# Performance work log

Measured on AMD Instinct MI355X. Metric: run time of the kernel, lower is better.

## Reference

```python
import jax, jax.numpy as jnp
import numpy as np

B, C, H, W = 8, 512, 32, 32
NH = 8


def setup_inputs() -> dict:
    key = jax.random.key(0)
    ks = jax.random.split(key, 10)
    s = 1.0 / np.sqrt(C)
    return {
        "query": jax.random.normal(ks[0], (B, C, H, W), jnp.float32),
        "key": jax.random.normal(ks[1], (B, C, H, W), jnp.float32),
        "Wq": jax.random.normal(ks[2], (C, C), jnp.float32) * s,
        "bq": jnp.zeros((C,), jnp.float32),
        "Wk": jax.random.normal(ks[3], (C, C), jnp.float32) * s,
        "bk": jnp.zeros((C,), jnp.float32),
        "Wv": jax.random.normal(ks[4], (C, C), jnp.float32) * s,
        "bv": jnp.zeros((C,), jnp.float32),
        "Wo": jax.random.normal(ks[5], (C, C), jnp.float32) * s,
        "bo": jnp.zeros((C,), jnp.float32),
        "num_heads": NH,
    }


def reference(query, key, Wq, bq, Wk, bk, Wv, bv, Wo, bo, num_heads):
    b, c, h, w = query.shape
    hd = c // num_heads
    scale = hd ** (-0.5)
    # [B,C,H,W] -> [B, L, C] with L = H*W
    qf = jnp.transpose(query, (0, 2, 3, 1)).reshape(b, -1, c)
    kf = jnp.transpose(key, (0, 2, 3, 1)).reshape(b, -1, c)
    L = qf.shape[1]
    # Linear projections (torch Linear: x @ W.T + b); value = key
    q = qf @ Wq.T + bq
    k = kf @ Wk.T + bk
    v = kf @ Wv.T + bv
    # split heads: [B, L, NH, hd] -> [B, NH, L, hd]
    q = q.reshape(b, L, num_heads, hd).transpose(0, 2, 1, 3) * scale
    k = k.reshape(b, L, num_heads, hd).transpose(0, 2, 1, 3)
    v = v.reshape(b, L, num_heads, hd).transpose(0, 2, 1, 3)
    scores = jnp.einsum('bhqd,bhkd->bhqk', q, k)
    attn = jax.nn.softmax(scores, axis=-1)  # dropout p=0.0 -> identity
    o = jnp.einsum('bhqk,bhkd->bhqd', attn, v)
    o = o.transpose(0, 2, 1, 3).reshape(b, L, c)
    o = o @ Wo.T + bo
    o = o + qf + kf  # residual with flattened query and key
    return jnp.transpose(o.reshape(b, h, w, c), (0, 3, 1, 2))
```

## Files before the change

### kernel.cpp

```cpp
#include <hip/hip_runtime.h>
#include <stdint.h>

#define B_  8
#define C_  512
#define L_  1024
#define NH_ 8
#define HD_ 64

typedef __attribute__((ext_vector_type(8))) short short8;
typedef __attribute__((ext_vector_type(4))) short short4v;
typedef __attribute__((ext_vector_type(4))) float f32x4;
typedef __attribute__((ext_vector_type(2))) unsigned uint2v;

#define MFMA(a,b,c) __builtin_amdgcn_mfma_f32_16x16x32_bf16((a),(b),(c),0,0,0)
#define GLD16(g,l) __builtin_amdgcn_global_load_lds( \
    (const __attribute__((address_space(1))) void*)(g), \
    (__attribute__((address_space(3))) void*)(l), 16, 0, 0)

__device__ __forceinline__ unsigned short f2bf(float f) {
  union { float f; unsigned u; } x; x.f = f;
  unsigned r = x.u + 0x7FFFu + ((x.u >> 16) & 1u);
  return (unsigned short)(r >> 16);
}

__device__ __forceinline__ unsigned cvtpk_bf16(float lo, float hi) {
  unsigned r;
  asm("v_cvt_pk_bf16_f32 %0, %1, %2" : "=v"(r) : "v"(lo), "v"(hi));
  return r;
}

__global__ __launch_bounds__(256) void k_transpose(
    const float* __restrict__ q, const float* __restrict__ k,
    unsigned short* __restrict__ qf, unsigned short* __restrict__ kf,
    const float* __restrict__ w0, const float* __restrict__ w1,
    const float* __restrict__ w2, const float* __restrict__ w3,
    unsigned short* __restrict__ wdst) {
  const int z = blockIdx.z;
  if (z == 16) {
    const int gb = blockIdx.y * 32 + blockIdx.x;
    const float* s = (gb < 128) ? w0 : (gb < 256) ? w1 : (gb < 384) ? w2 : w3;
    const int off = (gb & 127) * 2048 + threadIdx.x * 8;
    float4 v0 = *(const float4*)&s[off];
    float4 v1 = *(const float4*)&s[off + 4];
    short8 p;
    p[0] = (short)f2bf(v0.x); p[1] = (short)f2bf(v0.y);
    p[2] = (short)f2bf(v0.z); p[3] = (short)f2bf(v0.w);
    p[4] = (short)f2bf(v1.x); p[5] = (short)f2bf(v1.y);
    p[6] = (short)f2bf(v1.z); p[7] = (short)f2bf(v1.w);
    *(short8*)&wdst[(size_t)(gb >> 7) * 262144 + off] = p;
    return;
  }
  __shared__ float t[32][33];
  const int b = z >> 1;
  const float* src = (z & 1) ? k : q;
  unsigned short* dst = (z & 1) ? kf : qf;
  const int tx = threadIdx.x & 31;
  const int ty = threadIdx.x >> 5;
  const int l0 = blockIdx.x * 32;
  const int c0 = blockIdx.y * 32;
#pragma unroll
  for (int i = 0; i < 4; ++i)
    t[ty + 8*i][tx] = src[((size_t)b * C_ + c0 + ty + 8*i) * L_ + l0 + tx];
  __syncthreads();
#pragma unroll
  for (int i = 0; i < 4; ++i)
    dst[((size_t)b * L_ + l0 + ty + 8*i) * C_ + c0 + tx] = f2bf(t[tx][ty + 8*i]);
}

template<int MREP>
__device__ __forceinline__ void gemm_core(
    const unsigned short* __restrict__ A, const unsigned short* __restrict__ W,
    const float* __restrict__ bias, void* __restrict__ outp,
    const float* __restrict__ resQ, const float* __restrict__ resK,
    int mode, float scale, unsigned short* lA, unsigned short* lB,
    int tm, int tn) {
  const int lane = threadIdx.x & 63;
  const int wid  = threadIdx.x >> 6;
  const int wm = wid >> 1, wn = wid & 1;
  const int r16 = lane & 15;
  const int g4  = lane >> 4;

  f32x4 acc[MREP][4];
#pragma unroll
  for (int i = 0; i < MREP; ++i)
#pragma unroll
    for (int j = 0; j < 4; ++j) acc[i][j] = (f32x4){0.f, 0.f, 0.f, 0.f};

  for (int kt = 0; kt < C_; kt += 64) {
#pragma unroll
    for (int i = 0; i < MREP; ++i) {
      int chunk = wid * MREP + i;
      int row = chunk * 8 + (lane >> 3);
      int col = (lane & 7) * 8;
      GLD16(A + (size_t)(tm + row) * C_ + kt + col, &lA[chunk * 512]);
    }
#pragma unroll
    for (int i = 0; i < 4; ++i) {
      int chunk = wid * 4 + i;
      int row = chunk * 8 + (lane >> 3);
      int col = (lane & 7) * 8;
      GLD16(W + (size_t)(tn + row) * C_ + kt + col, &lB[chunk * 512]);
    }
    __syncthreads();
#pragma unroll
    for (int ks = 0; ks < 2; ++ks) {
      const int co = ks * 32 + g4 * 8;
      short8 af[MREP], bw[4];
#pragma unroll
      for (int i = 0; i < MREP; ++i)
        af[i] = *(const short8*)&lA[(wm*(MREP*16) + i*16 + r16) * 64 + co];
#pragma unroll
      for (int j = 0; j < 4; ++j) bw[j] = *(const short8*)&lB[(wn*64 + j*16 + r16) * 64 + co];
#pragma unroll
      for (int i = 0; i < MREP; ++i)
#pragma unroll
        for (int j = 0; j < 4; ++j) acc[i][j] = MFMA(af[i], bw[j], acc[i][j]);
    }
    __syncthreads();
  }

  if (mode <= 1) {
    unsigned short* out = (unsigned short*)outp;
#pragma unroll
    for (int i = 0; i < MREP; ++i)
#pragma unroll
      for (int j = 0; j < 4; ++j) {
        int c = tn + wn*64 + j*16 + r16;
        float bia = bias[c];
        int h = c >> 6, d = c & 63;
#pragma unroll
        for (int r = 0; r < 4; ++r) {
          int gm = tm + wm*(MREP*16) + i*16 + g4*4 + r;
          int b = gm >> 10, l = gm & 1023;
          out[(((size_t)b * NH_ + h) * L_ + l) * HD_ + d] = f2bf((acc[i][j][r] + bia) * scale);
        }
      }
  } else if (mode == 2) {
    unsigned short* out = (unsigned short*)outp;
#pragma unroll
    for (int i = 0; i < MREP; ++i)
#pragma unroll
      for (int j = 0; j < 4; ++j) {
        int c = tn + wn*64 + j*16 + r16;
        float bia = bias[c];
        int h = c >> 6, d = c & 63;
        int gm0 = tm + wm*(MREP*16) + i*16 + g4*4;
        int b = gm0 >> 10, l0 = gm0 & 1023;
        short4v pk;
#pragma unroll
        for (int r = 0; r < 4; ++r) pk[r] = (short)f2bf(acc[i][j][r] + bia);
        *(short4v*)&out[(((size_t)b * NH_ + h) * HD_ + d) * L_ + l0] = pk;
      }
  } else {
    float* out = (float*)outp;
#pragma unroll
    for (int i = 0; i < MREP; ++i)
#pragma unroll
      for (int j = 0; j < 4; ++j) {
        int c = tn + wn*64 + j*16 + r16;
        float bia = bias[c];
        int gm0 = tm + wm*(MREP*16) + i*16 + g4*4;
        int b = gm0 >> 10, l0 = gm0 & 1023;
        size_t idx = ((size_t)b * C_ + c) * L_ + l0;
        float4 q4 = *(const float4*)&resQ[idx];
        float4 k4 = *(const float4*)&resK[idx];
        float4 o4;
        o4.x = acc[i][j][0] + bia + q4.x + k4.x;
        o4.y = acc[i][j][1] + bia + q4.y + k4.y;
        o4.z = acc[i][j][2] + bia + q4.z + k4.z;
        o4.w = acc[i][j][3] + bia + q4.w + k4.w;
        *(float4*)&out[idx] = o4;
      }
  }
}

__global__ __launch_bounds__(256) void k_proj(
    const unsigned short* __restrict__ qf, const unsigned short* __restrict__ kf,
    const unsigned short* __restrict__ Wqb, const unsigned short* __restrict__ Wkb,
    const unsigned short* __restrict__ Wvb,
    const float* __restrict__ bq, const float* __restrict__ bk, const float* __restrict__ bv,
    unsigned short* __restrict__ Qw, unsigned short* __restrict__ Kw,
    unsigned short* __restrict__ VTw) {
  __shared__ unsigned short lA[128 * 64];
  __shared__ unsigned short lB[128 * 64];
  const int bid = blockIdx.x;
  const int xcd = bid & 7;
  const int i_  = bid >> 3;
  const int ml  = i_ / 12;
  const int rem = i_ - ml * 12;
  const int z   = rem >> 2;
  const int n   = rem & 3;
  const int m   = xcd * 8 + ml;
  const unsigned short* A = (z == 0) ? qf : kf;
  const unsigned short* W = (z == 0) ? Wqb : (z == 1) ? Wkb : Wvb;
  const float* bias = (z == 0) ? bq : (z == 1) ? bk : bv;
  void* out = (z == 0) ? (void*)Qw : (z == 1) ? (void*)Kw : (void*)VTw;
  float scale = (z == 0) ? 0.125f * 1.44269504088896f : 1.0f;
  gemm_core<4>(A, W, bias, out, nullptr, nullptr, z, scale, lA, lB, m * 128, n * 128);
}

__global__ __launch_bounds__(256) void k_outproj(
    const unsigned short* __restrict__ O, const unsigned short* __restrict__ Wob,
    const float* __restrict__ bo, float* __restrict__ out,
    const float* __restrict__ query, const float* __restrict__ key) {
  __shared__ unsigned short lA[64 * 64];
  __shared__ unsigned short lB[128 * 64];
  const int bid = blockIdx.x;
  const int xcd = bid & 7;
  const int i_  = bid >> 3;
  const int m   = xcd * 16 + (i_ >> 2);
  const int n   = i_ & 3;
  gemm_core<2>(O, Wob, bo, out, query, key, 3, 1.0f, lA, lB, m * 64, n * 128);
}

__global__ __launch_bounds__(256, 2) void k_attn(
    const unsigned short* __restrict__ Q, const unsigned short* __restrict__ K,
    const unsigned short* __restrict__ VT, unsigned short* __restrict__ O) {
  __shared__ unsigned short Kt[2][64 * 64];
  __shared__ unsigned short Vt[2][64 * 64];
  const int lane = threadIdx.x & 63;
  const int wid  = threadIdx.x >> 6;
  const int bid  = blockIdx.x;
  const int xcd  = bid & 7;
  const int i_   = bid >> 3;
  const int bh   = xcd * 8 + (i_ >> 3);
  const int qb   = i_ & 7;
  const int qrow0 = qb * 128 + wid * 32;
  const int r16 = lane & 15;
  const int g4  = lane >> 4;
  const size_t base = (size_t)bh * L_ * HD_;
  const unsigned short* Kg = K + base;
  const unsigned short* Vg = VT + base;

  const int s0 = wid * 128 + lane;
  const int row0 = s0 >> 3,        ch0 = (s0 & 7) ^ (row0 & 7);
  const int row1 = (s0 + 64) >> 3, ch1 = ((s0 + 64) & 7) ^ (row1 & 7);

#define STAGE_KV(nxt, kt0) { \
    GLD16(Kg + (size_t)((kt0) + row0) * HD_ + ch0 * 8, &Kt[nxt][(wid*128)*8]); \
    GLD16(Kg + (size_t)((kt0) + row1) * HD_ + ch1 * 8, &Kt[nxt][(wid*128+64)*8]); \
    GLD16(Vg + (size_t)row0 * L_ + (kt0) + ch0 * 8, &Vt[nxt][(wid*128)*8]); \
    GLD16(Vg + (size_t)row1 * L_ + (kt0) + ch1 * 8, &Vt[nxt][(wid*128+64)*8]); \
  }

  short8 qv[2][2];
#pragma unroll
  for (int i = 0; i < 2; ++i)
#pragma unroll
    for (int ks = 0; ks < 2; ++ks)
      qv[i][ks] = *(const short8*)(Q + base + (size_t)(qrow0 + i*16 + r16) * HD_ + ks*32 + g4*8);

  short8 vones;
#pragma unroll
  for (int e = 0; e < 8; ++e) vones[e] = (short)0x3F80;

  f32x4 lacc[2];
  f32x4 oacc[2][4];
#pragma unroll
  for (int i = 0; i < 2; ++i) {
    lacc[i] = (f32x4){0.f, 0.f, 0.f, 0.f};
#pragma unroll
    for (int j = 0; j < 4; ++j) oacc[i][j] = (f32x4){0.f, 0.f, 0.f, 0.f};
  }

  STAGE_KV(0, 0);
  __syncthreads();

  int cur = 0;
  for (int t = 0; t < 16; ++t) {
    if (t < 15) STAGE_KV(cur ^ 1, (t + 1) * 64);

    const unsigned short* lK = &Kt[cur][0];
    const unsigned short* lV = &Vt[cur][0];

    f32x4 sc[2][4];
#pragma unroll
    for (int i = 0; i < 2; ++i)
#pragma unroll
      for (int cf = 0; cf < 4; ++cf) sc[i][cf] = (f32x4){0.f, 0.f, 0.f, 0.f};

    __builtin_amdgcn_s_setprio(1);
#pragma unroll
    for (int cf = 0; cf < 4; ++cf) {
      const int h = cf >> 1, c = cf & 1;
      const int rr = h*32 + ((r16 >> 2) << 3) + ((r16 & 3) << 1) + c;
      const int s  = ((r16 & 3) << 1) + c;
      const int rowb = rr * 64;
      short8 kb0 = *(const short8*)&lK[rowb + ((g4) ^ s) * 8];
      short8 kb1 = *(const short8*)&lK[rowb + ((4 + g4) ^ s) * 8];
      sc[0][cf] = MFMA(kb0, qv[0][0], sc[0][cf]);
      sc[0][cf] = MFMA(kb1, qv[0][1], sc[0][cf]);
      sc[1][cf] = MFMA(kb0, qv[1][0], sc[1][cf]);
      sc[1][cf] = MFMA(kb1, qv[1][1], sc[1][cf]);
    }
    __builtin_amdgcn_s_setprio(0);

    const int swz = r16 & 7;
#pragma unroll
    for (int h = 0; h < 2; ++h) {
      union { unsigned u[4]; short8 s8; } pu0, pu1;
#pragma unroll
      for (int r = 0; r < 4; ++r) {
        pu0.u[r] = cvtpk_bf16(exp2f(sc[0][h*2][r]), exp2f(sc[0][h*2+1][r]));
        pu1.u[r] = cvtpk_bf16(exp2f(sc[1][h*2][r]), exp2f(sc[1][h*2+1][r]));
      }
      short8 pa0 = pu0.s8;
      short8 pa1 = pu1.s8;
      __builtin_amdgcn_s_setprio(1);
      lacc[0] = MFMA(pa0, vones, lacc[0]);
      lacc[1] = MFMA(pa1, vones, lacc[1]);
#pragma unroll
      for (int j = 0; j < 4; ++j) {
        short8 vb = *(const short8*)&lV[(j*16 + r16) * 64 + ((h*4 + g4) ^ swz) * 8];
        oacc[0][j] = MFMA(pa0, vb, oacc[0][j]);
        oacc[1][j] = MFMA(pa1, vb, oacc[1][j]);
      }
      __builtin_amdgcn_s_setprio(0);
    }

    __syncthreads();
    cur ^= 1;
  }

  const int b = bh >> 3, h = bh & 7;
#pragma unroll
  for (int i = 0; i < 2; ++i) {
    float linv[4];
#pragma unroll
    for (int r = 0; r < 4; ++r) linv[r] = 1.0f / lacc[i][r];
#pragma unroll
    for (int j = 0; j < 4; ++j)
#pragma unroll
      for (int r = 0; r < 4; ++r) {
        int row = qrow0 + i*16 + g4*4 + r;
        int col = h*64 + j*16 + r16;
        O[((size_t)b * L_ + row) * C_ + col] = f2bf(oacc[i][j][r] * linv[r]);
      }
  }
#undef STAGE_KV
}

extern "C" void kernel_launch(void* const* d_in, const int* in_sizes, int n_in,
                              void* d_out, int out_size, void* d_ws, size_t ws_size,
                              hipStream_t stream) {
  (void)in_sizes; (void)n_in; (void)out_size; (void)ws_size;
  const float* query = (const float*)d_in[0];
  const float* key   = (const float*)d_in[1];
  const float* Wq = (const float*)d_in[2];
  const float* bq = (const float*)d_in[3];
  const float* Wk = (const float*)d_in[4];
  const float* bk = (const float*)d_in[5];
  const float* Wv = (const float*)d_in[6];
  const float* bv = (const float*)d_in[7];
  const float* Wo = (const float*)d_in[8];
  const float* bo = (const float*)d_in[9];

  char* ws = (char*)d_ws;
  unsigned short* qf  = (unsigned short*)(ws);
  unsigned short* kf  = (unsigned short*)(ws + 8388608);
  unsigned short* Wqb = (unsigned short*)(ws + 16777216);
  unsigned short* Wkb = Wqb + 262144;
  unsigned short* Wvb = Wkb + 262144;
  unsigned short* Wob = Wvb + 262144;
  unsigned short* Qw  = (unsigned short*)(ws + 18874368);
  unsigned short* Kw  = (unsigned short*)(ws + 27262976);
  unsigned short* VTw = (unsigned short*)(ws + 35651584);
  unsigned short* Ow  = (unsigned short*)(ws + 44040192);

  k_transpose<<<dim3(32, 16, 17), 256, 0, stream>>>(query, key, qf, kf,
                                                    Wq, Wk, Wv, Wo, Wqb);
  k_proj<<<dim3(768), 256, 0, stream>>>(qf, kf, Wqb, Wkb, Wvb, bq, bk, bv, Qw, Kw, VTw);
  k_attn<<<dim3(512), 256, 0, stream>>>(Qw, Kw, VTw, Ow);
  k_outproj<<<dim3(512), 256, 0, stream>>>(Ow, Wob, bo, (float*)d_out, query, key);
}
```

Before: 93.04 us.

## Double-buffer GEMM LDS tiles with swizzled layout and prefetch next K-slice

```diff
diff --git a/kernel.cpp b/kernel.cpp
--- a/kernel.cpp
+++ b/kernel.cpp
@@ -80,44 +80,64 @@
   const int r16 = lane & 15;
   const int g4  = lane >> 4;
 
+  constexpr int ASLOTS = MREP * 128;
+  constexpr int BSLOTS = 512;
+
+  const int sB0 = wid * 128 + lane;
+  const int rB0 = sB0 >> 2;
+  const int cB0 = (sB0 & 3) ^ ((rB0 >> 1) & 3);
+  const int sA0 = wid * (ASLOTS / 4) + lane;
+  const int rA0 = sA0 >> 2;
+  const int cA0 = (sA0 & 3) ^ ((rA0 >> 1) & 3);
+
+#define G_STAGE(bb, kt) { \
+    if constexpr (MREP == 4) { \
+      GLD16(A + (size_t)(tm + rA0) * C_ + (kt) + cA0 * 8, &lA[(bb)*ASLOTS*8 + (wid*128)*8]); \
+      GLD16(A + (size_t)(tm + rA0 + 16) * C_ + (kt) + cA0 * 8, &lA[(bb)*ASLOTS*8 + (wid*128+64)*8]); \
+    } else { \
+      GLD16(A + (size_t)(tm + rA0) * C_ + (kt) + cA0 * 8, &lA[(bb)*ASLOTS*8 + (wid*64)*8]); \
+    } \
+    GLD16(W + (size_t)(tn + rB0) * C_ + (kt) + cB0 * 8, &lB[(bb)*BSLOTS*8 + (wid*128)*8]); \
+    GLD16(W + (size_t)(tn + rB0 + 16) * C_ + (kt) + cB0 * 8, &lB[(bb)*BSLOTS*8 + (wid*128+64)*8]); \
+  }
+
   f32x4 acc[MREP][4];
 #pragma unroll
   for (int i = 0; i < MREP; ++i)
 #pragma unroll
     for (int j = 0; j < 4; ++j) acc[i][j] = (f32x4){0.f, 0.f, 0.f, 0.f};
 
-  for (int kt = 0; kt < C_; kt += 64) {
+  G_STAGE(0, 0);
+  __syncthreads();
+
+  int cur = 0;
+  for (int t = 0; t < 16; ++t) {
+    if (t < 15) G_STAGE(cur ^ 1, (t + 1) * 32);
+
+    const unsigned short* cAb = &lA[cur * ASLOTS * 8];
+    const unsigned short* cBb = &lB[cur * BSLOTS * 8];
+    short8 af[MREP], bw[4];
 #pragma unroll
     for (int i = 0; i < MREP; ++i) {
-      int chunk = wid * MREP + i;
-      int row = chunk * 8 + (lane >> 3);
-      int col = (lane & 7) * 8;
-      GLD16(A + (size_t)(tm + row) * C_ + kt + col, &lA[chunk * 512]);
+      int row = wm * (MREP * 16) + i * 16 + r16;
+      af[i] = *(const short8*)&cAb[(row * 4 + (g4 ^ ((row >> 1) & 3))) * 8];
     }
 #pragma unroll
-    for (int i = 0; i < 4; ++i) {
-      int chunk = wid * 4 + i;
-      int row = chunk * 8 + (lane >> 3);
-      int col = (lane & 7) * 8;
-      GLD16(W + (size_t)(tn + row) * C_ + kt + col, &lB[chunk * 512]);
+    for (int j = 0; j < 4; ++j) {
+      int row = wn * 64 + j * 16 + r16;
+      bw[j] = *(const short8*)&cBb[(row * 4 + (g4 ^ ((row >> 1) & 3))) * 8];
     }
+    __builtin_amdgcn_s_setprio(1);
+#pragma unroll
+    for (int i = 0; i < MREP; ++i)
+#pragma unroll
+      for (int j = 0; j < 4; ++j) acc[i][j] = MFMA(af[i], bw[j], acc[i][j]);
+    __builtin_amdgcn_s_setprio(0);
+
     __syncthreads();
-#pragma unroll
-    for (int ks = 0; ks < 2; ++ks) {
-      const int co = ks * 32 + g4 * 8;
-      short8 af[MREP], bw[4];
-#pragma unroll
-      for (int i = 0; i < MREP; ++i)
-        af[i] = *(const short8*)&lA[(wm*(MREP*16) + i*16 + r16) * 64 + co];
-#pragma unroll
-      for (int j = 0; j < 4; ++j) bw[j] = *(const short8*)&lB[(wn*64 + j*16 + r16) * 64 + co];
-#pragma unroll
-      for (int i = 0; i < MREP; ++i)
-#pragma unroll
-        for (int j = 0; j < 4; ++j) acc[i][j] = MFMA(af[i], bw[j], acc[i][j]);
-    }
-    __syncthreads();
-  }
+    cur ^= 1;
+  }
+#undef G_STAGE
 
   if (mode <= 1) {
     unsigned short* out = (unsigned short*)outp;
@@ -181,8 +201,8 @@
     const float* __restrict__ bq, const float* __restrict__ bk, const float* __restrict__ bv,
     unsigned short* __restrict__ Qw, unsigned short* __restrict__ Kw,
     unsigned short* __restrict__ VTw) {
-  __shared__ unsigned short lA[128 * 64];
-  __shared__ unsigned short lB[128 * 64];
+  __shared__ unsigned short lA[2 * 512 * 8];
+  __shared__ unsigned short lB[2 * 512 * 8];
   const int bid = blockIdx.x;
   const int xcd = bid & 7;
   const int i_  = bid >> 3;
@@ -203,8 +223,8 @@
     const unsigned short* __restrict__ O, const unsigned short* __restrict__ Wob,
     const float* __restrict__ bo, float* __restrict__ out,
     const float* __restrict__ query, const float* __restrict__ key) {
-  __shared__ unsigned short lA[64 * 64];
-  __shared__ unsigned short lB[128 * 64];
+  __shared__ unsigned short lA[2 * 256 * 8];
+  __shared__ unsigned short lB[2 * 512 * 8];
   const int bid = blockIdx.x;
   const int xcd = bid & 7;
   const int i_  = bid >> 3;
```

Result: no change. 94.09 us (+1.1%).
